# Kernel tuning notes

Hardware: AMD Instinct MI355X
Metric: run time of the kernel (lower is better)

Reference implementation:

```python
import jax, jax.numpy as jnp
import numpy as np

N_NODES = 100000
N_EDGES = 1600000
NFEAT = 512
NHID = 64
NCLASS = 40


def setup_inputs() -> dict:
    key = jax.random.key(0)
    ks = jax.random.split(key, 8)
    x = jax.random.normal(ks[0], (N_NODES, NFEAT), dtype=jnp.float32)
    edge_row = jax.random.randint(ks[1], (N_EDGES,), 0, N_NODES, dtype=jnp.int32)
    edge_col = jax.random.randint(ks[2], (N_EDGES,), 0, N_NODES, dtype=jnp.int32)
    # normalized adjacency values (positive, small, like D^-1/2 A D^-1/2 entries)
    adj_vals = jax.random.uniform(ks[3], (N_EDGES,), dtype=jnp.float32) * 0.1
    # Glorot-style init as in Kipf's GraphConvolution reset_parameters
    W1 = jax.random.uniform(ks[4], (NFEAT, NHID), dtype=jnp.float32,
                            minval=-1.0, maxval=1.0) / jnp.sqrt(jnp.float32(NHID))
    b1 = jax.random.uniform(ks[5], (NHID,), dtype=jnp.float32,
                            minval=-1.0, maxval=1.0) / jnp.sqrt(jnp.float32(NHID))
    W10 = jax.random.uniform(ks[6], (NHID, NCLASS), dtype=jnp.float32,
                             minval=-1.0, maxval=1.0) / jnp.sqrt(jnp.float32(NCLASS))
    b10 = jax.random.uniform(ks[7], (NCLASS,), dtype=jnp.float32,
                             minval=-1.0, maxval=1.0) / jnp.sqrt(jnp.float32(NCLASS))
    return {"x": x, "adj_vals": adj_vals, "W1": W1, "b1": b1,
            "W10": W10, "b10": b10,
            "edge_row": edge_row, "edge_col": edge_col}


def reference(x, adj_vals, W1, b1, W10, b10, edge_row, edge_col):
    def spmm(vals, feat):
        # sparse adj (COO) @ dense feat: gather source rows, scale, scatter-add to dest
        msgs = vals[:, None] * feat[edge_col]          # [E, d]
        return jax.ops.segment_sum(msgs, edge_row, num_segments=N_NODES)

    # gc1: support = x @ W1; out = spmm(adj, support) + b1
    h = spmm(adj_vals, x @ W1) + b1                    # [N, NHID]
    h = jax.nn.relu(h)
    # dropout: eval mode -> identity
    # gc10
    out = spmm(adj_vals, h @ W10) + b10                # [N, NCLASS]
    return jax.nn.log_softmax(out, axis=1)
```

## Files before the change

kernel.cpp:

```cpp
#include <hip/hip_runtime.h>

#define NND 100000
#define NE  1600000
#define NF  512
#define NH  64
#define NC  40

#define BROWS 256
#define NB ((NND + BROWS - 1) / BROWS)
#define BCAP 4864
#define EPB 8192
#define NEB ((NE + EPB - 1) / EPB)
#define W10PAD 52
#define HPAD 68

typedef unsigned short u16;
typedef unsigned int   u32;
typedef __attribute__((ext_vector_type(8))) __bf16 bf16x8;
typedef __attribute__((ext_vector_type(8))) u16    u16x8;
typedef __attribute__((ext_vector_type(4))) float  f32x4;

__device__ __forceinline__ u16 f2bf(float f) {
  u32 u = __builtin_bit_cast(u32, f);
  u += 0x7FFFu + ((u >> 16) & 1u);
  return (u16)(u >> 16);
}
__device__ __forceinline__ u32 pack2(float a, float b) {
  return (u32)f2bf(a) | ((u32)f2bf(b) << 16);
}
__device__ __forceinline__ float bf2f(u16 h) {
  return __builtin_bit_cast(float, (u32)h << 16);
}
__device__ __forceinline__ bf16x8 pack8(const float4& a, const float4& b) {
  uint4 v;
  v.x = pack2(a.x, a.y); v.y = pack2(a.z, a.w);
  v.z = pack2(b.x, b.y); v.w = pack2(b.z, b.w);
  return __builtin_bit_cast(bf16x8, v);
}

__global__ __launch_bounds__(256) void w1t_k(const float* __restrict__ W1,
                                             u16* __restrict__ w1t,
                                             int* __restrict__ gcursor) {
  if (blockIdx.x == 0) {
    for (int i = threadIdx.x; i < NB; i += 256) gcursor[i] = 0;
  }
  int i = blockIdx.x * 256 + threadIdx.x;
  if (i >= NF * NH) return;
  int n = i >> 9, k = i & 511;
  w1t[i] = f2bf(W1[(size_t)k * NH + n]);
}

__global__ __launch_bounds__(256) void gemm1_k(const float* __restrict__ x,
                                               const u16* __restrict__ w1t,
                                               u16* __restrict__ out) {
  __shared__ u16 Bs[2][64][72];
  const int t = threadIdx.x, w = t >> 6, lane = t & 63;
  const int l15 = lane & 15, l4 = lane >> 4;
  const int rowBase = blockIdx.x * 128;
  const int r0 = rowBase + w * 32 + l15;
  const float* pa0 = x + (size_t)min(r0, NND - 1) * NF + l4 * 8;
  const float* pa1 = x + (size_t)min(r0 + 16, NND - 1) * NF + l4 * 8;

  f32x4 acc[2][4];
#pragma unroll
  for (int i = 0; i < 2; ++i)
#pragma unroll
    for (int j = 0; j < 4; ++j) acc[i][j] = (f32x4){0.f, 0.f, 0.f, 0.f};

  uint4  bR[2];
  float4 aR[2][2][2];

  auto issueB = [&](int k0) {
#pragma unroll
    for (int i = 0; i < 2; ++i) {
      int c = t + i * 256;
      bR[i] = *(const uint4*)(w1t + (size_t)(c >> 3) * NF + k0 + (c & 7) * 8);
    }
  };
  auto issueA = [&](int k0) {
#pragma unroll
    for (int s = 0; s < 2; ++s) {
      const float* q0 = pa0 + k0 + s * 32;
      const float* q1 = pa1 + k0 + s * 32;
      aR[0][s][0] = *(const float4*)(q0);
      aR[0][s][1] = *(const float4*)(q0 + 4);
      aR[1][s][0] = *(const float4*)(q1);
      aR[1][s][1] = *(const float4*)(q1 + 4);
    }
  };

  issueB(0);
  issueA(0);
  for (int it = 0; it < 8; ++it) {
    const int b = it & 1;
#pragma unroll
    for (int i = 0; i < 2; ++i) {
      int c = t + i * 256;
      *(uint4*)&Bs[b][c >> 3][(c & 7) * 8] = bR[i];
    }
    bf16x8 fa0[2], fa1[2];
#pragma unroll
    for (int s = 0; s < 2; ++s) {
      fa0[s] = pack8(aR[0][s][0], aR[0][s][1]);
      fa1[s] = pack8(aR[1][s][0], aR[1][s][1]);
    }
    if (it < 7) { issueB((it + 1) * 64); issueA((it + 1) * 64); }
    __syncthreads();
#pragma unroll
    for (int s = 0; s < 2; ++s) {
#pragma unroll
      for (int ct = 0; ct < 4; ++ct) {
        bf16x8 bb = *(const bf16x8*)&Bs[b][ct * 16 + l15][s * 32 + l4 * 8];
        acc[0][ct] = __builtin_amdgcn_mfma_f32_16x16x32_bf16(fa0[s], bb, acc[0][ct], 0, 0, 0);
        acc[1][ct] = __builtin_amdgcn_mfma_f32_16x16x32_bf16(fa1[s], bb, acc[1][ct], 0, 0, 0);
      }
    }
  }

#pragma unroll
  for (int rt = 0; rt < 2; ++rt)
#pragma unroll
    for (int ct = 0; ct < 4; ++ct)
#pragma unroll
      for (int i = 0; i < 4; ++i) {
        int row = rowBase + w * 32 + rt * 16 + l4 * 4 + i;
        if (row < NND) out[(size_t)row * NH + ct * 16 + l15] = f2bf(acc[rt][ct][i]);
      }
}

__global__ __launch_bounds__(1024) void bscatter_k(const float* __restrict__ vals,
                                                   const int* __restrict__ rows,
                                                   const int* __restrict__ cols,
                                                   int* __restrict__ gcursor,
                                                   int2* __restrict__ eb1) {
  __shared__ int cnt[NB];
  __shared__ int base[NB];
  const int t = threadIdx.x;
  for (int i = t; i < NB; i += 1024) cnt[i] = 0;
  __syncthreads();
  const int gb = blockIdx.x * EPB;
  int bin[8], rnk[8], rr[8], cc[8];
  float vv[8];
#pragma unroll
  for (int k = 0; k < 8; ++k) {
    int i = gb + t + k * 1024;
    if (i < NE) {
      rr[k] = rows[i]; cc[k] = cols[i]; vv[k] = vals[i];
      bin[k] = rr[k] >> 8;
      rnk[k] = atomicAdd(&cnt[bin[k]], 1);
    } else bin[k] = -1;
  }
  __syncthreads();
  for (int i = t; i < NB; i += 1024)
    if (cnt[i]) base[i] = i * BCAP + atomicAdd(&gcursor[i], cnt[i]);
  __syncthreads();
#pragma unroll
  for (int k = 0; k < 8; ++k) {
    if (bin[k] >= 0) {
      int pos = base[bin[k]] + rnk[k];
      eb1[pos] = make_int2((int)(((u32)cc[k] << 8) | (u32)(rr[k] & 255)),
                           __float_as_int(vv[k]));
    }
  }
}

__global__ __launch_bounds__(1024) void spmm1f_k(const int* __restrict__ gcursor,
                                                 const int2* __restrict__ eb1,
                                                 const u16* __restrict__ s1,
                                                 const float* __restrict__ b1,
                                                 const float* __restrict__ W10,
                                                 u16* __restrict__ s2,
                                                 int2* __restrict__ eb2,
                                                 int* __restrict__ rowoff,
                                                 int* __restrict__ rowcnt) {
  __shared__ int2 se[BCAP];
  __shared__ u16 w10s[64 * W10PAD];
  __shared__ int cnt[BROWS];
  __shared__ int sc[BROWS];
  __shared__ int wsum[4];
  const int bkt = blockIdx.x, t = threadIdx.x;
  const int w = t >> 6, lane = t & 63;
  const int half = lane >> 5, fl = lane & 31;
  const int nE = min(gcursor[bkt], BCAP);
  const int beg = bkt * BCAP;
  for (int i = t; i < 64 * W10PAD; i += 1024) {
    int k = i / W10PAD, c = i - k * W10PAD;
    w10s[i] = (c < NC) ? f2bf(W10[k * NC + c]) : (u16)0;
  }
  if (t < BROWS) cnt[t] = 0;
  __syncthreads();
  int2 mye[5]; int myrow[5], myrank[5];
#pragma unroll
  for (int k = 0; k < 5; ++k) {
    int i = t + k * 1024;
    myrow[k] = -1;
    if (i < nE) {
      int2 e = eb1[beg + i];
      mye[k] = e;
      myrow[k] = e.x & 255;
      myrank[k] = atomicAdd(&cnt[myrow[k]], 1);
    }
  }
  __syncthreads();
  int c0 = 0, inc = 0;
  if (t < BROWS) {
    c0 = cnt[t]; inc = c0;
#pragma unroll
    for (int off = 1; off < 64; off <<= 1) {
      int u = __shfl_up(inc, off, 64);
      if ((t & 63) >= off) inc += u;
    }
    if ((t & 63) == 63) wsum[t >> 6] = inc;
  }
  __syncthreads();
  if (t < BROWS) {
    int pre = 0;
#pragma unroll
    for (int k = 0; k < 4; ++k) pre += (k < (t >> 6)) ? wsum[k] : 0;
    int ex = pre + inc - c0;
    sc[t] = ex;
    rowoff[bkt * BROWS + t] = beg + ex;
    rowcnt[bkt * BROWS + t] = c0;
  }
  __syncthreads();
#pragma unroll
  for (int k = 0; k < 5; ++k)
    if (myrow[k] >= 0)
      se[sc[myrow[k]] + myrank[k]] = make_int2((int)((u32)mye[k].x >> 8), mye[k].y);
  __syncthreads();

#pragma unroll
  for (int k = 0; k < 5; ++k) {
    int i = t + k * 1024;
    if (i < nE) eb2[beg + i] = se[i];
  }

  const float2 bias2 = *(const float2*)(b1 + fl * 2);
  u32 hpack[16];
#pragma unroll 1
  for (int i = 0; i < 16; ++i) {
    int r8 = w * 16 + i;
    int s = sc[r8], n = cnt[r8];
    float a0 = 0.f, a1 = 0.f, a2 = 0.f, a3 = 0.f;
    float a4 = 0.f, a5 = 0.f, a6 = 0.f, a7 = 0.f;
    int j = 0;
    for (; j + 7 < n; j += 8) {
      int2 e0 = se[s + j + half];
      int2 e1 = se[s + j + 2 + half];
      int2 e2 = se[s + j + 4 + half];
      int2 e3 = se[s + j + 6 + half];
      u32 f0 = *(const u32*)(s1 + (size_t)e0.x * NH + fl * 2);
      u32 f1 = *(const u32*)(s1 + (size_t)e1.x * NH + fl * 2);
      u32 f2 = *(const u32*)(s1 + (size_t)e2.x * NH + fl * 2);
      u32 f3 = *(const u32*)(s1 + (size_t)e3.x * NH + fl * 2);
      float v0 = __int_as_float(e0.y), v1 = __int_as_float(e1.y);
      float v2 = __int_as_float(e2.y), v3 = __int_as_float(e3.y);
      a0 = fmaf(v0, bf2f((u16)f0), a0);
      a1 = fmaf(v0, bf2f((u16)(f0 >> 16)), a1);
      a2 = fmaf(v1, bf2f((u16)f1), a2);
      a3 = fmaf(v1, bf2f((u16)(f1 >> 16)), a3);
      a4 = fmaf(v2, bf2f((u16)f2), a4);
      a5 = fmaf(v2, bf2f((u16)(f2 >> 16)), a5);
      a6 = fmaf(v3, bf2f((u16)f3), a6);
      a7 = fmaf(v3, bf2f((u16)(f3 >> 16)), a7);
    }
    for (; j + 3 < n; j += 4) {
      int2 e0 = se[s + j + half];
      int2 e1 = se[s + j + 2 + half];
      u32 f0 = *(const u32*)(s1 + (size_t)e0.x * NH + fl * 2);
      u32 f1 = *(const u32*)(s1 + (size_t)e1.x * NH + fl * 2);
      float v0 = __int_as_float(e0.y), v1 = __int_as_float(e1.y);
      a0 = fmaf(v0, bf2f((u16)f0), a0);
      a1 = fmaf(v0, bf2f((u16)(f0 >> 16)), a1);
      a2 = fmaf(v1, bf2f((u16)f1), a2);
      a3 = fmaf(v1, bf2f((u16)(f1 >> 16)), a3);
    }
    for (; j < n; j += 2) {
      int idx = j + half;
      bool ok = idx < n;
      int2 e = se[s + (ok ? idx : 0)];
      float v = ok ? __int_as_float(e.y) : 0.f;
      u32 f = *(const u32*)(s1 + (size_t)e.x * NH + fl * 2);
      a0 = fmaf(v, bf2f((u16)f), a0);
      a1 = fmaf(v, bf2f((u16)(f >> 16)), a1);
    }
    float t0 = (a0 + a2) + (a4 + a6);
    float t1 = (a1 + a3) + (a5 + a7);
    t0 += __shfl_xor(t0, 32, 64);
    t1 += __shfl_xor(t1, 32, 64);
    hpack[i] = pack2(fmaxf(t0 + bias2.x, 0.f), fmaxf(t1 + bias2.y, 0.f));
  }
  __syncthreads();

  u16* hl = (u16*)se + (size_t)w * 16 * HPAD;
  if (half == 0) {
#pragma unroll
    for (int i = 0; i < 16; ++i) *(u32*)&hl[i * HPAD + fl * 2] = hpack[i];
  }

  const int l15 = lane & 15, l4 = lane >> 4;
  bf16x8 afr[2];
  afr[0] = *(const bf16x8*)&hl[l15 * HPAD + l4 * 8];
  afr[1] = *(const bf16x8*)&hl[l15 * HPAD + 32 + l4 * 8];

  f32x4 acc[3];
#pragma unroll
  for (int ct = 0; ct < 3; ++ct) acc[ct] = (f32x4){0.f, 0.f, 0.f, 0.f};
#pragma unroll
  for (int ct = 0; ct < 3; ++ct) {
#pragma unroll
    for (int kk = 0; kk < 2; ++kk) {
      u16x8 bw;
#pragma unroll
      for (int j = 0; j < 8; ++j)
        bw[j] = w10s[(kk * 32 + l4 * 8 + j) * W10PAD + ct * 16 + l15];
      acc[ct] = __builtin_amdgcn_mfma_f32_16x16x32_bf16(
          afr[kk], __builtin_bit_cast(bf16x8, bw), acc[ct], 0, 0, 0);
    }
  }
#pragma unroll
  for (int ct = 0; ct < 3; ++ct) {
    int c = ct * 16 + l15;
#pragma unroll
    for (int i = 0; i < 4; ++i) {
      int grow = bkt * BROWS + w * 16 + l4 * 4 + i;
      if (c < NC && grow < NND) s2[(size_t)grow * NC + c] = f2bf(acc[ct][i]);
    }
  }
}

__global__ __launch_bounds__(512) void spmm2h_k(const int2* __restrict__ eb2,
                                                const int* __restrict__ rowoff,
                                                const int* __restrict__ rowcnt,
                                                const u16* __restrict__ s2,
                                                const float* __restrict__ b10,
                                                float* __restrict__ out) {
  __shared__ int2 se[BCAP];
  __shared__ int roff[128];
  __shared__ int rcnt[128];
  const int bh = blockIdx.x;
  const int bkt = bh >> 1, bhalf = bh & 1;
  const int t = threadIdx.x, w = t >> 6, lane = t & 63;
  const int half = lane >> 5, fl = lane & 31;
  const bool act = fl < (NC / 2);
  const int fo = act ? fl * 2 : 0;
  const int rowBase = bkt * BROWS + bhalf * 128;
  if (t < 128) {
    roff[t] = rowoff[rowBase + t];
    rcnt[t] = rowcnt[rowBase + t];
  }
  __syncthreads();
  const int base = roff[0];
  const int nE = min(roff[127] + rcnt[127] - base, BCAP);
  for (int i = t; i < nE; i += 512) se[i] = eb2[base + i];
  __syncthreads();

  const float2 bias2 = act ? *(const float2*)(b10 + fo) : make_float2(0.f, 0.f);
#pragma unroll 1
  for (int i = 0; i < 16; ++i) {
    int r8 = w * 16 + i;
    int s = roff[r8] - base, n = rcnt[r8];
    float a0 = 0.f, a1 = 0.f, a2 = 0.f, a3 = 0.f;
    float a4 = 0.f, a5 = 0.f, a6 = 0.f, a7 = 0.f;
    int j = 0;
    for (; j + 7 < n; j += 8) {
      int2 e0 = se[s + j + half];
      int2 e1 = se[s + j + 2 + half];
      int2 e2 = se[s + j + 4 + half];
      int2 e3 = se[s + j + 6 + half];
      u32 f0 = *(const u32*)(s2 + (size_t)e0.x * NC + fo);
      u32 f1 = *(const u32*)(s2 + (size_t)e1.x * NC + fo);
      u32 f2 = *(const u32*)(s2 + (size_t)e2.x * NC + fo);
      u32 f3 = *(const u32*)(s2 + (size_t)e3.x * NC + fo);
      float v0 = __int_as_float(e0.y), v1 = __int_as_float(e1.y);
      float v2 = __int_as_float(e2.y), v3 = __int_as_float(e3.y);
      a0 = fmaf(v0, bf2f((u16)f0), a0);
      a1 = fmaf(v0, bf2f((u16)(f0 >> 16)), a1);
      a2 = fmaf(v1, bf2f((u16)f1), a2);
      a3 = fmaf(v1, bf2f((u16)(f1 >> 16)), a3);
      a4 = fmaf(v2, bf2f((u16)f2), a4);
      a5 = fmaf(v2, bf2f((u16)(f2 >> 16)), a5);
      a6 = fmaf(v3, bf2f((u16)f3), a6);
      a7 = fmaf(v3, bf2f((u16)(f3 >> 16)), a7);
    }
    for (; j + 3 < n; j += 4) {
      int2 e0 = se[s + j + half];
      int2 e1 = se[s + j + 2 + half];
      u32 f0 = *(const u32*)(s2 + (size_t)e0.x * NC + fo);
      u32 f1 = *(const u32*)(s2 + (size_t)e1.x * NC + fo);
      float v0 = __int_as_float(e0.y), v1 = __int_as_float(e1.y);
      a0 = fmaf(v0, bf2f((u16)f0), a0);
      a1 = fmaf(v0, bf2f((u16)(f0 >> 16)), a1);
      a2 = fmaf(v1, bf2f((u16)f1), a2);
      a3 = fmaf(v1, bf2f((u16)(f1 >> 16)), a3);
    }
    for (; j < n; j += 2) {
      int idx = j + half;
      bool ok = idx < n;
      int2 e = se[s + (ok ? idx : 0)];
      float v = ok ? __int_as_float(e.y) : 0.f;
      u32 f = *(const u32*)(s2 + (size_t)e.x * NC + fo);
      a0 = fmaf(v, bf2f((u16)f), a0);
      a1 = fmaf(v, bf2f((u16)(f >> 16)), a1);
    }
    float t0 = (a0 + a2) + (a4 + a6);
    float t1 = (a1 + a3) + (a5 + a7);
    t0 += __shfl_xor(t0, 32, 64);
    t1 += __shfl_xor(t1, 32, 64);
    int grow = rowBase + r8;
    if (grow >= NND) continue;
    float v0 = act ? t0 + bias2.x : -INFINITY;
    float v1 = act ? t1 + bias2.y : -INFINITY;
    float m = fmaxf(v0, v1);
#pragma unroll
    for (int o = 16; o; o >>= 1) m = fmaxf(m, __shfl_xor(m, o, 64));
    float e0 = act ? __expf(v0 - m) : 0.f;
    float e1 = act ? __expf(v1 - m) : 0.f;
    float ss = e0 + e1;
#pragma unroll
    for (int o = 16; o; o >>= 1) ss += __shfl_xor(ss, o, 64);
    float l = __logf(ss);
    if (act && half == 0)
      *(float2*)(out + (size_t)grow * NC + fo) = make_float2(v0 - m - l, v1 - m - l);
  }
}

extern "C" void kernel_launch(void* const* d_in, const int* in_sizes, int n_in,
                              void* d_out, int out_size, void* d_ws, size_t ws_size,
                              hipStream_t stream) {
  const float* x    = (const float*)d_in[0];
  const float* adj  = (const float*)d_in[1];
  const float* W1   = (const float*)d_in[2];
  const float* b1   = (const float*)d_in[3];
  const float* W10  = (const float*)d_in[4];
  const float* b10  = (const float*)d_in[5];
  const int*   erow = (const int*)d_in[6];
  const int*   ecol = (const int*)d_in[7];
  float* out = (float*)d_out;

  char* p = (char*)d_ws;
  u16*  s1  = (u16*)p;    p += (size_t)NND * NH * 2;
  u16*  s2  = (u16*)p;    p += (size_t)NND * NC * 2;
  u16*  w1t = (u16*)p;    p += (size_t)NF * NH * 2;
  int2* eb1 = (int2*)p;   p += (size_t)NB * BCAP * 8;
  int2* eb2 = (int2*)p;   p += (size_t)NB * BCAP * 8;
  int* rowoff = (int*)p;  p += (size_t)NB * BROWS * 4;
  int* rowcnt = (int*)p;  p += (size_t)NB * BROWS * 4;
  int* gcursor = (int*)p;

  w1t_k<<<(NF * NH + 255) / 256, 256, 0, stream>>>(W1, w1t, gcursor);
  bscatter_k<<<NEB, 1024, 0, stream>>>(adj, erow, ecol, gcursor, eb1);

  gemm1_k<<<(NND + 127) / 128, 256, 0, stream>>>(x, w1t, s1);
  spmm1f_k<<<NB, 1024, 0, stream>>>(gcursor, eb1, s1, b1, W10, s2, eb2, rowoff, rowcnt);
  spmm2h_k<<<NB * 2, 512, 0, stream>>>(eb2, rowoff, rowcnt, s2, b10, out);
}
```

Baseline: 165.8 us.

## Stage binned edges in shared memory for coalesced bucket scatter writes

The edge bucketing kernel now does a block-wide prefix scan over bin counts and first places edges in shared memory in bin-sorted order. It then writes them to the global buckets so that consecutive threads write consecutive addresses within each bin, replacing fully random 8-byte stores. Edges per block are halved so the staging buffer fits in LDS. This doubles the number of blocks and the global cursor atomics, and adds two extra barriers and the scan.

```diff
diff --git a/kernel.cpp b/kernel.cpp
--- a/kernel.cpp
+++ b/kernel.cpp
@@ -9,7 +9,7 @@
 #define BROWS 256
 #define NB ((NND + BROWS - 1) / BROWS)
 #define BCAP 4864
-#define EPB 8192
+#define EPB 4096
 #define NEB ((NE + EPB - 1) / EPB)
 #define W10PAD 52
 #define HPAD 68
@@ -133,16 +133,20 @@
                                                    const int* __restrict__ cols,
                                                    int* __restrict__ gcursor,
                                                    int2* __restrict__ eb1) {
+  __shared__ int2 sedg[EPB];
+  __shared__ u16  sbin[EPB];
   __shared__ int cnt[NB];
-  __shared__ int base[NB];
+  __shared__ int lstart[NB];
+  __shared__ int gbase[NB];
+  __shared__ int wsum[7];
   const int t = threadIdx.x;
   for (int i = t; i < NB; i += 1024) cnt[i] = 0;
   __syncthreads();
   const int gb = blockIdx.x * EPB;
-  int bin[8], rnk[8], rr[8], cc[8];
-  float vv[8];
-#pragma unroll
-  for (int k = 0; k < 8; ++k) {
+  int bin[4], rnk[4], rr[4], cc[4];
+  float vv[4];
+#pragma unroll
+  for (int k = 0; k < 4; ++k) {
     int i = gb + t + k * 1024;
     if (i < NE) {
       rr[k] = rows[i]; cc[k] = cols[i]; vv[k] = vals[i];
@@ -151,15 +155,43 @@
     } else bin[k] = -1;
   }
   __syncthreads();
-  for (int i = t; i < NB; i += 1024)
-    if (cnt[i]) base[i] = i * BCAP + atomicAdd(&gcursor[i], cnt[i]);
-  __syncthreads();
-#pragma unroll
-  for (int k = 0; k < 8; ++k) {
+  int c0 = 0, inc = 0;
+  if (t < 448) {
+    c0 = (t < NB) ? cnt[t] : 0;
+    inc = c0;
+#pragma unroll
+    for (int off = 1; off < 64; off <<= 1) {
+      int u = __shfl_up(inc, off, 64);
+      if ((t & 63) >= off) inc += u;
+    }
+    if ((t & 63) == 63) wsum[t >> 6] = inc;
+  }
+  __syncthreads();
+  if (t < NB) {
+    int pre = 0;
+#pragma unroll
+    for (int k = 0; k < 7; ++k) pre += (k < (t >> 6)) ? wsum[k] : 0;
+    lstart[t] = pre + inc - c0;
+    if (c0) gbase[t] = t * BCAP + atomicAdd(&gcursor[t], c0);
+  }
+  __syncthreads();
+#pragma unroll
+  for (int k = 0; k < 4; ++k) {
     if (bin[k] >= 0) {
-      int pos = base[bin[k]] + rnk[k];
-      eb1[pos] = make_int2((int)(((u32)cc[k] << 8) | (u32)(rr[k] & 255)),
-                           __float_as_int(vv[k]));
+      int p = lstart[bin[k]] + rnk[k];
+      sedg[p] = make_int2((int)(((u32)cc[k] << 8) | (u32)(rr[k] & 255)),
+                          __float_as_int(vv[k]));
+      sbin[p] = (u16)bin[k];
+    }
+  }
+  __syncthreads();
+  const int nE = min(EPB, NE - gb);
+#pragma unroll
+  for (int k = 0; k < 4; ++k) {
+    int i = t + k * 1024;
+    if (i < nE) {
+      int b = sbin[i];
+      eb1[gbase[b] + (i - lstart[b])] = sedg[i];
     }
   }
 }
```

Result: no change. 163.8 us (-1.2%).
